# Optimization experiments

Measured on AMD Instinct MI355X. Metric: run time of the kernel, lower is better.

The kernel has to match this reference:

```python
import jax, jax.numpy as jnp
import numpy as np

TABLE_SZ = 2 ** 14
FEAT_DIM = 2
NUM_LEVELS = 16
MIN_RES = 16.0
MAX_RES = 512.0
B = 1 << 20

# corner order v0..v7 from get_nearest_vertices_coords (z-ascending, ccw)
OFFSETS = jnp.array([[0, 0, 0], [1, 0, 0], [1, 1, 0], [0, 1, 0],
                     [0, 0, 1], [1, 0, 1], [1, 1, 1], [0, 1, 1]], dtype=jnp.int32)


def setup_inputs() -> dict:
    key = jax.random.key(0)
    kx, kt = jax.random.split(key)
    x = jax.random.uniform(kx, (B, 3), dtype=jnp.float32)  # coords in [0,1)
    # RandomUniform(-1e-4, 1e-4) initializer for all 16 tables, stacked
    tables = jax.random.uniform(kt, (NUM_LEVELS, TABLE_SZ, FEAT_DIM),
                                dtype=jnp.float32, minval=-1e-4, maxval=1e-4)
    return {"x": x, "tables": tables}


def reference(x, tables):
    # per-level resolutions: floor(min_res * b**l), b geometric growth factor
    b = jnp.exp((jnp.log(MAX_RES) - jnp.log(MIN_RES)) / (NUM_LEVELS - 1))
    res = jnp.floor(MIN_RES * b ** jnp.arange(NUM_LEVELS, dtype=jnp.float32))  # [L]

    # NOTE: original computes interp weights from the UNSCALED position
    # (position - floor(position)); since x in [0,1) this equals x. Faithful.
    w = x - jnp.floor(x)  # [B,3]
    off = OFFSETS.astype(bool)[None]  # [1,8,3]
    # trilinear weight per corner: prod over xyz of (w if offset else 1-w)
    cw = jnp.prod(jnp.where(off, w[:, None, :], 1.0 - w[:, None, :]), axis=-1)  # [B,8]

    P1 = jnp.uint32(2654435761)
    P2 = jnp.uint32(805459861)
    TS = jnp.uint32(TABLE_SZ)

    def level(carry, lvl):
        table, r = lvl  # [T,F], scalar
        sp = r * x  # [B,3]
        low = jnp.floor(sp).astype(jnp.int32)
        high = jnp.ceil(sp).astype(jnp.int32)
        corners = jnp.where(off, high[:, None, :], low[:, None, :]).astype(jnp.uint32)  # [B,8,3]
        # spatial hash: x ^ (p1*y) ^ (p2*z) mod table_sz (uint32 wraparound;
        # table_sz is a power of two so this matches int32-wrap + floormod)
        h = (corners[..., 0] ^ (P1 * corners[..., 1]) ^ (P2 * corners[..., 2])) % TS
        feats = table[h.astype(jnp.int32)]  # gather -> [B,8,F]
        return carry, jnp.einsum('bkf,bk->bf', feats, cw)  # [B,F]

    _, outs = jax.lax.scan(level, None, (tables, res))  # [L,B,F]
    # matches tf.concat over levels along feature axis
    return jnp.transpose(outs, (1, 0, 2)).reshape(x.shape[0], NUM_LEVELS * FEAT_DIM)
```

## Files before the change

kernel.cpp:

```cpp
#include <hip/hip_runtime.h>
#include <cmath>

#define TABLE_SZ 16384
#define NLEV 16
#define HALF 8

struct ResArr { float r[NLEV]; };

__global__ __launch_bounds__(256) void cvt_tables(
    const float* __restrict__ src, uint32_t* __restrict__ dst, int n_entries)
{
    int i = blockIdx.x * blockDim.x + threadIdx.x;
    int e = i * 4;
    if (e + 3 < n_entries) {
        const float4* s4 = (const float4*)(src) + i * 2;
        float4 a = s4[0], b = s4[1];
        uint32_t o[4];
        float v[8] = {a.x,a.y,a.z,a.w,b.x,b.y,b.z,b.w};
        #pragma unroll
        for (int k = 0; k < 4; ++k) {
            uint32_t lo = __float_as_uint(v[2*k+0]);
            uint32_t hi = __float_as_uint(v[2*k+1]);
            lo = (lo + 0x7FFFu + ((lo >> 16) & 1u)) >> 16;
            hi = (hi + 0x7FFFu + ((hi >> 16) & 1u)) & 0xFFFF0000u;
            o[k] = lo | hi;
        }
        *(uint4*)(dst + e) = make_uint4(o[0], o[1], o[2], o[3]);
    }
}

template <int TBLOCK>
__device__ __forceinline__ void stage_bf(const uint32_t* __restrict__ tb, int l,
                                         uint32_t* buf, int tid, int wid)
{
    const char* gbase = (const char*)tb + (size_t)l * (TABLE_SZ * 4);
    #pragma unroll
    for (int j = 0; j < (TABLE_SZ * 4) / (TBLOCK * 16); ++j) {
        uint32_t goff = (uint32_t)(j * (TBLOCK * 16) + tid * 16);
        uint32_t loff = (uint32_t)(j * (TBLOCK * 16) + wid * 1024);
        __builtin_amdgcn_global_load_lds(
            (const __attribute__((address_space(1))) uint32_t*)(gbase + goff),
            (__attribute__((address_space(3))) uint32_t*)((char*)buf + loff),
            16, 0, 0);
    }
}

__device__ __forceinline__ float2 level_accum_bf(const uint32_t* tab, float r,
                                                 float px, float py, float pz,
                                                 const float* cw)
{
    const uint32_t P1 = 2654435761u, P2 = 805459861u;
    const uint32_t m  = TABLE_SZ - 1u;

    float sx = r*px, sy = r*py, sz = r*pz;
    uint32_t lx = (uint32_t)sx;
    uint32_t hx = (uint32_t)ceilf(sx);
    uint32_t ly = (uint32_t)sy;
    uint32_t hy = (uint32_t)ceilf(sy);
    uint32_t lz = (uint32_t)sz;
    uint32_t hz = (uint32_t)ceilf(sz);
    uint32_t yl = P1*ly, yh = P1*hy;
    uint32_t zl = P2*lz, zh = P2*hz;

    float a0, a1;
    {
        uint32_t v0 = tab[(lx ^ yl ^ zl) & m];
        uint32_t v1 = tab[(hx ^ yl ^ zl) & m];
        uint32_t v2 = tab[(hx ^ yh ^ zl) & m];
        uint32_t v3 = tab[(lx ^ yh ^ zl) & m];
        a0  = __uint_as_float(v0 << 16)         * cw[0];
        a1  = __uint_as_float(v0 & 0xFFFF0000u) * cw[0];
        a0 += __uint_as_float(v1 << 16)         * cw[1];
        a1 += __uint_as_float(v1 & 0xFFFF0000u) * cw[1];
        a0 += __uint_as_float(v2 << 16)         * cw[2];
        a1 += __uint_as_float(v2 & 0xFFFF0000u) * cw[2];
        a0 += __uint_as_float(v3 << 16)         * cw[3];
        a1 += __uint_as_float(v3 & 0xFFFF0000u) * cw[3];
    }
    {
        uint32_t v4 = tab[(lx ^ yl ^ zh) & m];
        uint32_t v5 = tab[(hx ^ yl ^ zh) & m];
        uint32_t v6 = tab[(hx ^ yh ^ zh) & m];
        uint32_t v7 = tab[(lx ^ yh ^ zh) & m];
        a0 += __uint_as_float(v4 << 16)         * cw[4];
        a1 += __uint_as_float(v4 & 0xFFFF0000u) * cw[4];
        a0 += __uint_as_float(v5 << 16)         * cw[5];
        a1 += __uint_as_float(v5 & 0xFFFF0000u) * cw[5];
        a0 += __uint_as_float(v6 << 16)         * cw[6];
        a1 += __uint_as_float(v6 & 0xFFFF0000u) * cw[6];
        a0 += __uint_as_float(v7 << 16)         * cw[7];
        a1 += __uint_as_float(v7 & 0xFFFF0000u) * cw[7];
    }
    return make_float2(a0, a1);
}

template <int TBLOCK, int TPPT>
__global__ __launch_bounds__(TBLOCK) void mrhe_db(
    const float* __restrict__ x,
    const uint32_t* __restrict__ tb,
    float* __restrict__ out,
    ResArr res, int B)
{
    constexpr int ROUNDS = (TABLE_SZ * 4) / (TBLOCK * 16);
    static_assert(ROUNDS == 4 || ROUNDS == 8 || ROUNDS == 16, "vmcnt literal");

    __shared__ uint32_t tab[2][TABLE_SZ];

    const int tid  = threadIdx.x;
    const int wid  = tid >> 6;
    const int base = blockIdx.x * (TBLOCK * TPPT);

    float px[TPPT], py[TPPT], pz[TPPT];
    float cw[TPPT][8];
    #pragma unroll
    for (int p = 0; p < TPPT; ++p) {
        int idx = base + p * TBLOCK + tid;
        size_t j = (idx < B) ? (size_t)idx : 0;
        px[p] = x[3*j+0]; py[p] = x[3*j+1]; pz[p] = x[3*j+2];
        float ax = 1.0f - px[p], ay = 1.0f - py[p], az = 1.0f - pz[p];
        cw[p][0] = (ax*ay)*az;
        cw[p][1] = (px[p]*ay)*az;
        cw[p][2] = (px[p]*py[p])*az;
        cw[p][3] = (ax*py[p])*az;
        cw[p][4] = (ax*ay)*pz[p];
        cw[p][5] = (px[p]*ay)*pz[p];
        cw[p][6] = (px[p]*py[p])*pz[p];
        cw[p][7] = (ax*py[p])*pz[p];
    }

    stage_bf<TBLOCK>(tb, 0, tab[0], tid, wid);

    float o[TPPT][2*HALF];

    #pragma unroll
    for (int l = 0; l < NLEV; ++l) {
        if (l + 1 < NLEV) {
            stage_bf<TBLOCK>(tb, l + 1, tab[(l + 1) & 1], tid, wid);
            if constexpr (ROUNDS == 4)
                asm volatile("s_waitcnt vmcnt(4)" ::: "memory");
            else if constexpr (ROUNDS == 8)
                asm volatile("s_waitcnt vmcnt(8)" ::: "memory");
            else
                asm volatile("s_waitcnt vmcnt(16)" ::: "memory");
        } else {
            asm volatile("s_waitcnt vmcnt(0)" ::: "memory");
        }
        asm volatile("s_barrier" ::: "memory");

        const float r = res.r[l];
        const uint32_t* buf = tab[l & 1];
        #pragma unroll
        for (int p = 0; p < TPPT; ++p) {
            float2 a = level_accum_bf(buf, r, px[p], py[p], pz[p], cw[p]);
            o[p][2*(l & 7) + 0] = a.x;
            o[p][2*(l & 7) + 1] = a.y;
        }

        if ((l & 7) == 7) {
            const int half = l >> 3;
            #pragma unroll
            for (int p = 0; p < TPPT; ++p) {
                int idx = base + p * TBLOCK + tid;
                if (idx < B) {
                    float* po = out + (size_t)idx * (2*NLEV) + half * (2*HALF);
                    #pragma unroll
                    for (int j = 0; j < (2*HALF)/4; ++j) {
                        float4 v;
                        v.x = o[p][4*j+0]; v.y = o[p][4*j+1];
                        v.z = o[p][4*j+2]; v.w = o[p][4*j+3];
                        ((float4*)po)[j] = v;
                    }
                }
            }
        }

        asm volatile("s_barrier" ::: "memory");
    }
}

__global__ __launch_bounds__(256) void mrhe_direct(
    const float* __restrict__ x,
    const float* __restrict__ tables,
    float* __restrict__ out,
    ResArr res, int B)
{
    int i = blockIdx.x * blockDim.x + threadIdx.x;
    if (i >= B) return;
    float px = x[3*(size_t)i+0], py = x[3*(size_t)i+1], pz = x[3*(size_t)i+2];
    float ax = 1.0f - px, ay = 1.0f - py, az = 1.0f - pz;
    float cw[8] = {(ax*ay)*az,(px*ay)*az,(px*py)*az,(ax*py)*az,
                   (ax*ay)*pz,(px*ay)*pz,(px*py)*pz,(ax*py)*pz};
    const uint32_t P1 = 2654435761u, P2 = 805459861u, m = TABLE_SZ - 1u;
    float o[2*NLEV];
    #pragma unroll
    for (int l = 0; l < NLEV; ++l) {
        float r = res.r[l];
        float sx = r*px, sy = r*py, sz = r*pz;
        uint32_t lx = (uint32_t)sx, hx = (uint32_t)ceilf(sx);
        uint32_t ly = (uint32_t)sy, hy = (uint32_t)ceilf(sy);
        uint32_t lz = (uint32_t)sz, hz = (uint32_t)ceilf(sz);
        uint32_t yl = P1*ly, yh = P1*hy, zl = P2*lz, zh = P2*hz;
        uint32_t h[8] = {(lx^yl^zl)&m,(hx^yl^zl)&m,(hx^yh^zl)&m,(lx^yh^zl)&m,
                         (lx^yl^zh)&m,(hx^yl^zh)&m,(hx^yh^zh)&m,(lx^yh^zh)&m};
        const float2* tbl = (const float2*)tables + (size_t)l * TABLE_SZ;
        float a0 = 0.f, a1 = 0.f;
        #pragma unroll
        for (int k = 0; k < 8; ++k) {
            float2 f = tbl[h[k]];
            a0 += f.x * cw[k]; a1 += f.y * cw[k];
        }
        o[2*l+0] = a0; o[2*l+1] = a1;
    }
    float4* po = (float4*)(out + (size_t)i * (2*NLEV));
    #pragma unroll
    for (int j = 0; j < (2*NLEV)/4; ++j) {
        float4 v; v.x = o[4*j+0]; v.y = o[4*j+1]; v.z = o[4*j+2]; v.w = o[4*j+3];
        po[j] = v;
    }
}

extern "C" void kernel_launch(void* const* d_in, const int* in_sizes, int n_in,
                              void* d_out, int out_size, void* d_ws, size_t ws_size,
                              hipStream_t stream)
{
    const float* x      = (const float*)d_in[0];
    const float* tables = (const float*)d_in[1];
    float* out = (float*)d_out;
    int B = in_sizes[0] / 3;

    ResArr res;
    float bgrow = expf((logf(512.0f) - logf(16.0f)) / 15.0f);
    for (int l = 0; l < NLEV; ++l)
        res.r[l] = floorf(16.0f * powf(bgrow, (float)l));

    const int n_entries = NLEV * TABLE_SZ;
    const size_t need = (size_t)n_entries * 4;

    if (ws_size >= need && d_ws) {
        uint32_t* tb = (uint32_t*)d_ws;
        hipLaunchKernelGGL(cvt_tables, dim3(n_entries/4/256), dim3(256), 0, stream,
                           tables, tb, n_entries);

        hipFuncAttributes attr{};
        hipError_t e = hipFuncGetAttributes(&attr, (const void*)mrhe_db<1024, 1>);
        bool use1024 = (e == hipSuccess) && (attr.localSizeBytes == 0);

        if (use1024) {
            int per_block = 1024 * 1;
            int grid = (B + per_block - 1) / per_block;
            hipLaunchKernelGGL((mrhe_db<1024, 1>), dim3(grid), dim3(1024), 0, stream,
                               x, tb, out, res, B);
        } else {
            int per_block = 512 * 2;
            int grid = (B + per_block - 1) / per_block;
            hipLaunchKernelGGL((mrhe_db<512, 2>), dim3(grid), dim3(512), 0, stream,
                               x, tb, out, res, B);
        }
    } else {
        int grid = (B + 255) / 256;
        hipLaunchKernelGGL(mrhe_direct, dim3(grid), dim3(256), 0, stream,
                           x, tables, out, res, B);
    }
}
```

Baseline: 108.1 us.

## Split levels between LDS-staged tables and direct global gathers for fine levels

Adds a hybrid kernel with 512-thread blocks. It stages only the first 11 levels' bf16 tables into LDS with double buffering. The five finest levels (11-15) are gathered straight from the fp32 global tables and interleaved with the LDS levels, so their loads overlap the staging traffic. This cuts per-block LDS staging volume and barrier rounds, at the cost of scattered global gathers that rely on the L2 cache and of extra register pressure for buffered outputs. The fine levels now use fp32 table values instead of bf16.

After: 171.3 us. 1.58x slower.

```diff
diff --git a/kernel.cpp b/kernel.cpp
--- a/kernel.cpp
+++ b/kernel.cpp
@@ -3,7 +3,8 @@
 
 #define TABLE_SZ 16384
 #define NLEV 16
-#define HALF 8
+#define BLOCK 512
+#define NLDS 11
 
 struct ResArr { float r[NLEV]; };
 
@@ -45,53 +46,138 @@
     }
 }
 
+struct C8 { uint32_t h[8]; };
+__device__ __forceinline__ C8 corner_idx(float r, float px, float py, float pz)
+{
+    const uint32_t P1 = 2654435761u, P2 = 805459861u;
+    const uint32_t m  = TABLE_SZ - 1u;
+    float sx = r*px, sy = r*py, sz = r*pz;
+    uint32_t lx = (uint32_t)sx,  hx = (uint32_t)ceilf(sx);
+    uint32_t ly = (uint32_t)sy,  hy = (uint32_t)ceilf(sy);
+    uint32_t lz = (uint32_t)sz,  hz = (uint32_t)ceilf(sz);
+    uint32_t yl = P1*ly, yh = P1*hy, zl = P2*lz, zh = P2*hz;
+    C8 c;
+    c.h[0] = (lx ^ yl ^ zl) & m;
+    c.h[1] = (hx ^ yl ^ zl) & m;
+    c.h[2] = (hx ^ yh ^ zl) & m;
+    c.h[3] = (lx ^ yh ^ zl) & m;
+    c.h[4] = (lx ^ yl ^ zh) & m;
+    c.h[5] = (hx ^ yl ^ zh) & m;
+    c.h[6] = (hx ^ yh ^ zh) & m;
+    c.h[7] = (lx ^ yh ^ zh) & m;
+    return c;
+}
+
 __device__ __forceinline__ float2 level_accum_bf(const uint32_t* tab, float r,
                                                  float px, float py, float pz,
                                                  const float* cw)
 {
-    const uint32_t P1 = 2654435761u, P2 = 805459861u;
-    const uint32_t m  = TABLE_SZ - 1u;
-
-    float sx = r*px, sy = r*py, sz = r*pz;
-    uint32_t lx = (uint32_t)sx;
-    uint32_t hx = (uint32_t)ceilf(sx);
-    uint32_t ly = (uint32_t)sy;
-    uint32_t hy = (uint32_t)ceilf(sy);
-    uint32_t lz = (uint32_t)sz;
-    uint32_t hz = (uint32_t)ceilf(sz);
-    uint32_t yl = P1*ly, yh = P1*hy;
-    uint32_t zl = P2*lz, zh = P2*hz;
-
-    float a0, a1;
-    {
-        uint32_t v0 = tab[(lx ^ yl ^ zl) & m];
-        uint32_t v1 = tab[(hx ^ yl ^ zl) & m];
-        uint32_t v2 = tab[(hx ^ yh ^ zl) & m];
-        uint32_t v3 = tab[(lx ^ yh ^ zl) & m];
-        a0  = __uint_as_float(v0 << 16)         * cw[0];
-        a1  = __uint_as_float(v0 & 0xFFFF0000u) * cw[0];
-        a0 += __uint_as_float(v1 << 16)         * cw[1];
-        a1 += __uint_as_float(v1 & 0xFFFF0000u) * cw[1];
-        a0 += __uint_as_float(v2 << 16)         * cw[2];
-        a1 += __uint_as_float(v2 & 0xFFFF0000u) * cw[2];
-        a0 += __uint_as_float(v3 << 16)         * cw[3];
-        a1 += __uint_as_float(v3 & 0xFFFF0000u) * cw[3];
-    }
-    {
-        uint32_t v4 = tab[(lx ^ yl ^ zh) & m];
-        uint32_t v5 = tab[(hx ^ yl ^ zh) & m];
-        uint32_t v6 = tab[(hx ^ yh ^ zh) & m];
-        uint32_t v7 = tab[(lx ^ yh ^ zh) & m];
-        a0 += __uint_as_float(v4 << 16)         * cw[4];
-        a1 += __uint_as_float(v4 & 0xFFFF0000u) * cw[4];
-        a0 += __uint_as_float(v5 << 16)         * cw[5];
-        a1 += __uint_as_float(v5 & 0xFFFF0000u) * cw[5];
-        a0 += __uint_as_float(v6 << 16)         * cw[6];
-        a1 += __uint_as_float(v6 & 0xFFFF0000u) * cw[6];
-        a0 += __uint_as_float(v7 << 16)         * cw[7];
-        a1 += __uint_as_float(v7 & 0xFFFF0000u) * cw[7];
+    C8 c = corner_idx(r, px, py, pz);
+    float a0 = 0.f, a1 = 0.f;
+    #pragma unroll
+    for (int k = 0; k < 8; ++k) {
+        uint32_t v = tab[c.h[k]];
+        a0 += __uint_as_float(v << 16)         * cw[k];
+        a1 += __uint_as_float(v & 0xFFFF0000u) * cw[k];
     }
     return make_float2(a0, a1);
+}
+
+__global__ __launch_bounds__(BLOCK) void mrhe_hyb(
+    const float* __restrict__ x,
+    const float* __restrict__ ftab,
+    const uint32_t* __restrict__ tb,
+    float* __restrict__ out,
+    ResArr res, int B)
+{
+    __shared__ uint32_t tab[2][TABLE_SZ];
+
+    const int tid = threadIdx.x;
+    const int wid = tid >> 6;
+    const int idx = blockIdx.x * BLOCK + tid;
+    const size_t j = (idx < B) ? (size_t)idx : 0;
+
+    const float px = x[3*j+0], py = x[3*j+1], pz = x[3*j+2];
+    const float ax = 1.0f - px, ay = 1.0f - py, az = 1.0f - pz;
+    float cw[8];
+    cw[0] = (ax*ay)*az;  cw[1] = (px*ay)*az;
+    cw[2] = (px*py)*az;  cw[3] = (ax*py)*az;
+    cw[4] = (ax*ay)*pz;  cw[5] = (px*ay)*pz;
+    cw[6] = (px*py)*pz;  cw[7] = (ax*py)*pz;
+
+    stage_bf<BLOCK>(tb, 0, tab[0], tid, wid);
+
+    float o[16];
+    float opre[6];
+
+    #pragma unroll
+    for (int l = 0; l < NLDS; ++l) {
+        if (l + 1 < NLDS) {
+            stage_bf<BLOCK>(tb, l + 1, tab[(l + 1) & 1], tid, wid);
+            asm volatile("s_waitcnt vmcnt(8)" ::: "memory");
+        } else {
+            asm volatile("s_waitcnt vmcnt(0)" ::: "memory");
+        }
+        asm volatile("s_barrier" ::: "memory");
+
+        float2 gf[8];
+        if (l >= 5 && l <= 9) {
+            const int g = l + 6;
+            C8 c = corner_idx(res.r[g], px, py, pz);
+            const float2* t = (const float2*)ftab + (size_t)g * TABLE_SZ;
+            #pragma unroll
+            for (int k = 0; k < 8; ++k) gf[k] = t[c.h[k]];
+        }
+
+        {
+            float2 a = level_accum_bf(tab[l & 1], res.r[l], px, py, pz, cw);
+            o[2*(l & 7) + 0] = a.x;
+            o[2*(l & 7) + 1] = a.y;
+        }
+
+        if (l >= 5 && l <= 9) {
+            const int g = l + 6;
+            float b0 = 0.f, b1 = 0.f;
+            #pragma unroll
+            for (int k = 0; k < 8; ++k) {
+                b0 += gf[k].x * cw[k];
+                b1 += gf[k].y * cw[k];
+            }
+            if (l <= 7) {
+                opre[2*(l-5) + 0] = b0;
+                opre[2*(l-5) + 1] = b1;
+            } else {
+                o[2*(g & 7) + 0] = b0;
+                o[2*(g & 7) + 1] = b1;
+            }
+        }
+
+        if (l == 7 && idx < B) {
+            float4* po = (float4*)(out + (size_t)idx * (2*NLEV));
+            #pragma unroll
+            for (int q = 0; q < 4; ++q) {
+                float4 v;
+                v.x = o[4*q+0]; v.y = o[4*q+1]; v.z = o[4*q+2]; v.w = o[4*q+3];
+                po[q] = v;
+            }
+        }
+        if (l == 8) {
+            o[6]  = opre[0]; o[7]  = opre[1];
+            o[8]  = opre[2]; o[9]  = opre[3];
+            o[10] = opre[4]; o[11] = opre[5];
+        }
+        if (l == 10 && idx < B) {
+            float4* po = (float4*)(out + (size_t)idx * (2*NLEV) + 16);
+            #pragma unroll
+            for (int q = 0; q < 4; ++q) {
+                float4 v;
+                v.x = o[4*q+0]; v.y = o[4*q+1]; v.z = o[4*q+2]; v.w = o[4*q+3];
+                po[q] = v;
+            }
+        }
+
+        asm volatile("s_barrier" ::: "memory");
+    }
 }
 
 template <int TBLOCK, int TPPT>
@@ -102,7 +188,7 @@
     ResArr res, int B)
 {
     constexpr int ROUNDS = (TABLE_SZ * 4) / (TBLOCK * 16);
-    static_assert(ROUNDS == 4 || ROUNDS == 8 || ROUNDS == 16, "vmcnt literal");
+    static_assert(ROUNDS == 8, "vmcnt literal must match");
 
     __shared__ uint32_t tab[2][TABLE_SZ];
 
@@ -118,40 +204,30 @@
         size_t j = (idx < B) ? (size_t)idx : 0;
         px[p] = x[3*j+0]; py[p] = x[3*j+1]; pz[p] = x[3*j+2];
         float ax = 1.0f - px[p], ay = 1.0f - py[p], az = 1.0f - pz[p];
-        cw[p][0] = (ax*ay)*az;
-        cw[p][1] = (px[p]*ay)*az;
-        cw[p][2] = (px[p]*py[p])*az;
-        cw[p][3] = (ax*py[p])*az;
-        cw[p][4] = (ax*ay)*pz[p];
-        cw[p][5] = (px[p]*ay)*pz[p];
-        cw[p][6] = (px[p]*py[p])*pz[p];
-        cw[p][7] = (ax*py[p])*pz[p];
+        cw[p][0] = (ax*ay)*az;       cw[p][1] = (px[p]*ay)*az;
+        cw[p][2] = (px[p]*py[p])*az; cw[p][3] = (ax*py[p])*az;
+        cw[p][4] = (ax*ay)*pz[p];    cw[p][5] = (px[p]*ay)*pz[p];
+        cw[p][6] = (px[p]*py[p])*pz[p]; cw[p][7] = (ax*py[p])*pz[p];
     }
 
     stage_bf<TBLOCK>(tb, 0, tab[0], tid, wid);
 
-    float o[TPPT][2*HALF];
+    float o[TPPT][16];
 
     #pragma unroll
     for (int l = 0; l < NLEV; ++l) {
         if (l + 1 < NLEV) {
             stage_bf<TBLOCK>(tb, l + 1, tab[(l + 1) & 1], tid, wid);
-            if constexpr (ROUNDS == 4)
-                asm volatile("s_waitcnt vmcnt(4)" ::: "memory");
-            else if constexpr (ROUNDS == 8)
-                asm volatile("s_waitcnt vmcnt(8)" ::: "memory");
-            else
-                asm volatile("s_waitcnt vmcnt(16)" ::: "memory");
+            asm volatile("s_waitcnt vmcnt(8)" ::: "memory");
         } else {
             asm volatile("s_waitcnt vmcnt(0)" ::: "memory");
         }
         asm volatile("s_barrier" ::: "memory");
 
-        const float r = res.r[l];
         const uint32_t* buf = tab[l & 1];
         #pragma unroll
         for (int p = 0; p < TPPT; ++p) {
-            float2 a = level_accum_bf(buf, r, px[p], py[p], pz[p], cw[p]);
+            float2 a = level_accum_bf(buf, res.r[l], px[p], py[p], pz[p], cw[p]);
             o[p][2*(l & 7) + 0] = a.x;
             o[p][2*(l & 7) + 1] = a.y;
         }
@@ -162,13 +238,13 @@
             for (int p = 0; p < TPPT; ++p) {
                 int idx = base + p * TBLOCK + tid;
                 if (idx < B) {
-                    float* po = out + (size_t)idx * (2*NLEV) + half * (2*HALF);
+                    float* po = out + (size_t)idx * (2*NLEV) + half * 16;
                     #pragma unroll
-                    for (int j = 0; j < (2*HALF)/4; ++j) {
+                    for (int q = 0; q < 4; ++q) {
                         float4 v;
-                        v.x = o[p][4*j+0]; v.y = o[p][4*j+1];
-                        v.z = o[p][4*j+2]; v.w = o[p][4*j+3];
-                        ((float4*)po)[j] = v;
+                        v.x = o[p][4*q+0]; v.y = o[p][4*q+1];
+                        v.z = o[p][4*q+2]; v.w = o[p][4*q+3];
+                        ((float4*)po)[q] = v;
                     }
                 }
             }
@@ -190,32 +266,24 @@
     float ax = 1.0f - px, ay = 1.0f - py, az = 1.0f - pz;
     float cw[8] = {(ax*ay)*az,(px*ay)*az,(px*py)*az,(ax*py)*az,
                    (ax*ay)*pz,(px*ay)*pz,(px*py)*pz,(ax*py)*pz};
-    const uint32_t P1 = 2654435761u, P2 = 805459861u, m = TABLE_SZ - 1u;
     float o[2*NLEV];
     #pragma unroll
     for (int l = 0; l < NLEV; ++l) {
-        float r = res.r[l];
-        float sx = r*px, sy = r*py, sz = r*pz;
-        uint32_t lx = (uint32_t)sx, hx = (uint32_t)ceilf(sx);
-        uint32_t ly = (uint32_t)sy, hy = (uint32_t)ceilf(sy);
-        uint32_t lz = (uint32_t)sz, hz = (uint32_t)ceilf(sz);
-        uint32_t yl = P1*ly, yh = P1*hy, zl = P2*lz, zh = P2*hz;
-        uint32_t h[8] = {(lx^yl^zl)&m,(hx^yl^zl)&m,(hx^yh^zl)&m,(lx^yh^zl)&m,
-                         (lx^yl^zh)&m,(hx^yl^zh)&m,(hx^yh^zh)&m,(lx^yh^zh)&m};
+        C8 c = corner_idx(res.r[l], px, py, pz);
         const float2* tbl = (const float2*)tables + (size_t)l * TABLE_SZ;
         float a0 = 0.f, a1 = 0.f;
         #pragma unroll
         for (int k = 0; k < 8; ++k) {
-            float2 f = tbl[h[k]];
+            float2 f = tbl[c.h[k]];
             a0 += f.x * cw[k]; a1 += f.y * cw[k];
         }
         o[2*l+0] = a0; o[2*l+1] = a1;
     }
     float4* po = (float4*)(out + (size_t)i * (2*NLEV));
     #pragma unroll
-    for (int j = 0; j < (2*NLEV)/4; ++j) {
-        float4 v; v.x = o[4*j+0]; v.y = o[4*j+1]; v.z = o[4*j+2]; v.w = o[4*j+3];
-        po[j] = v;
+    for (int q = 0; q < (2*NLEV)/4; ++q) {
+        float4 v; v.x = o[4*q+0]; v.y = o[4*q+1]; v.z = o[4*q+2]; v.w = o[4*q+3];
+        po[q] = v;
     }
 }
 
@@ -242,14 +310,13 @@
                            tables, tb, n_entries);
 
         hipFuncAttributes attr{};
-        hipError_t e = hipFuncGetAttributes(&attr, (const void*)mrhe_db<1024, 1>);
-        bool use1024 = (e == hipSuccess) && (attr.localSizeBytes == 0);
-
-        if (use1024) {
-            int per_block = 1024 * 1;
-            int grid = (B + per_block - 1) / per_block;
-            hipLaunchKernelGGL((mrhe_db<1024, 1>), dim3(grid), dim3(1024), 0, stream,
-                               x, tb, out, res, B);
+        hipError_t e = hipFuncGetAttributes(&attr, (const void*)mrhe_hyb);
+        bool useHyb = (e == hipSuccess) && (attr.localSizeBytes == 0);
+
+        if (useHyb) {
+            int grid = (B + BLOCK - 1) / BLOCK;
+            hipLaunchKernelGGL(mrhe_hyb, dim3(grid), dim3(BLOCK), 0, stream,
+                               x, tables, tb, out, res, B);
         } else {
             int per_block = 512 * 2;
             int grid = (B + per_block - 1) / per_block;
```
